# Kernel tuning notes

Hardware: AMD Instinct MI355X
Metric: run time of the kernel (lower is better)

## Reference

```python
import jax, jax.numpy as jnp
import numpy as np

EPS = 1e-06

def _hermite_coeffs(coord_diff, sigmas):
    # coord_diff: [B,N,K,2], sigmas: [K] -> coeff: [B,N,K,6]
    dx = coord_diff[..., 0]  # [B,N,K]
    dy = coord_diff[..., 1]
    s2 = sigmas ** 2 + EPS   # [K], broadcasts over B,N
    s4 = sigmas ** 4 + EPS
    ones = jnp.ones_like(dx)
    # idx order follows nested (order, alpha) loop of the torch code:
    # (0,0), (0,1)->-dy, (1,0)->-dx, (0,2), (1,1), (2,0)
    coeff = jnp.stack([
        ones,
        -dy / s2,
        -dx / s2,
        dy ** 2 / s4 - 1.0 / s2,
        dx * dy / s4,
        dx ** 2 / s4 - 1.0 / s2,
    ], axis=-1)  # [B,N,K,6]
    return coeff


def setup_inputs() -> dict:
    key = jax.random.key(0)
    k1, k2, k3, k4, k5 = jax.random.split(key, 5)
    B, N, K, H, O = 4, 65536, 32, 6, 31
    return {
        "mlp_output": jax.random.normal(k1, (B, N, O), dtype=jnp.float32),
        "coord_diff": jax.random.normal(k2, (B, N, K, 2), dtype=jnp.float32),
        "sigmas": jax.random.uniform(k3, (K,), dtype=jnp.float32, minval=0.1, maxval=1.0),
        "gaussian_weights": jax.random.uniform(k4, (B, N, K), dtype=jnp.float32),
        "rbf_weights": jax.random.normal(k5, (K, H, O), dtype=jnp.float32),
    }


def reference(mlp_output, coord_diff, sigmas, gaussian_weights, rbf_weights):
    # final[b,n,o] = mlp_output[b,n,o] * sum_{k,h} coeff[b,n,k,h]*gw[b,n,k]*W[k,h,o]
    coeff = _hermite_coeffs(coord_diff, sigmas)            # [B,N,K,6]
    mix = jnp.einsum('bnkh,bnk,kho->bno', coeff, gaussian_weights, rbf_weights)
    return mlp_output * mix
```

## Files before the change

kernel.cpp:

```cpp
#include <hip/hip_runtime.h>

#define KK 32
#define HH 6
#define OO 31
#define OP 32
#define KT 8
#define EPS 1e-6f

#define W_DW (KK * HH * OP)
#define PTS_BLK 512
#define MIX_DW (PTS_BLK * OO)

__global__ __launch_bounds__(256, 2) void hermite_fused_kernel(
    const float* __restrict__ mlp,
    const float* __restrict__ cd,
    const float* __restrict__ sigmas,
    const float* __restrict__ gw,
    const float* __restrict__ W,
    float* __restrict__ out,
    int P)
{
    __shared__ float smem[MIX_DW];
    __shared__ float s_i2[KK];
    __shared__ float s_i4[KK];

    const int tid = threadIdx.x;
    if (tid < KK) {
        float s = sigmas[tid];
        s_i2[tid] = 1.0f / (s * s + EPS);
        s_i4[tid] = 1.0f / (s * s * s * s + EPS);
    }

    for (int j = tid; j < W_DW; j += 256) {
        int k = j / (HH * OP);
        int r = j - k * (HH * OP);
        int h = r >> 5;
        int o = r & 31;
        smem[j] = (o < OO) ? W[k * (HH * OO) + h * OO + o] : 0.0f;
    }
    __syncthreads();

    const int pA = blockIdx.x * PTS_BLK + tid;
    const float4* __restrict__ cdA = (const float4*)(cd + (size_t)pA * (KK * 2));
    const float4* __restrict__ cdB = cdA + (256 * KK * 2) / 4;
    const float4* __restrict__ gwA = (const float4*)(gw + (size_t)pA * KK);
    const float4* __restrict__ gwB = gwA + (256 * KK) / 4;

    float accA[OP], accB[OP];
#pragma unroll
    for (int o = 0; o < OP; ++o) { accA[o] = 0.0f; accB[o] = 0.0f; }

#pragma unroll 1
    for (int kt = 0; kt < KK / KT; ++kt) {
        float cA[KT * 2], cB[KT * 2], gA[KT], gB[KT];
#pragma unroll
        for (int i = 0; i < KT / 2; ++i) {
            float4 t = cdA[kt * (KT / 2) + i];
            cA[4 * i + 0] = t.x; cA[4 * i + 1] = t.y; cA[4 * i + 2] = t.z; cA[4 * i + 3] = t.w;
        }
#pragma unroll
        for (int i = 0; i < KT / 2; ++i) {
            float4 t = cdB[kt * (KT / 2) + i];
            cB[4 * i + 0] = t.x; cB[4 * i + 1] = t.y; cB[4 * i + 2] = t.z; cB[4 * i + 3] = t.w;
        }
#pragma unroll
        for (int i = 0; i < KT / 4; ++i) {
            float4 t = gwA[kt * (KT / 4) + i];
            gA[4 * i + 0] = t.x; gA[4 * i + 1] = t.y; gA[4 * i + 2] = t.z; gA[4 * i + 3] = t.w;
        }
#pragma unroll
        for (int i = 0; i < KT / 4; ++i) {
            float4 t = gwB[kt * (KT / 4) + i];
            gB[4 * i + 0] = t.x; gB[4 * i + 1] = t.y; gB[4 * i + 2] = t.z; gB[4 * i + 3] = t.w;
        }

#pragma unroll
        for (int j = 0; j < KT; ++j) {
            const int k = kt * KT + j;
            float i2 = s_i2[k];
            float i4 = s_i4[k];

            float dxA = cA[2 * j], dyA = cA[2 * j + 1], ga = gA[j];
            float t2A = ga * i2, t4A = ga * i4;
            float dxt4A = dxA * t4A, dyt4A = dyA * t4A;
            float d0A = ga;
            float d1A = -dyA * t2A;
            float d2A = -dxA * t2A;
            float d3A = fmaf(dyA, dyt4A, -t2A);
            float d4A = dxA * dyt4A;
            float d5A = fmaf(dxA, dxt4A, -t2A);

            float dxB = cB[2 * j], dyB = cB[2 * j + 1], gb = gB[j];
            float t2B = gb * i2, t4B = gb * i4;
            float dxt4B = dxB * t4B, dyt4B = dyB * t4B;
            float d0B = gb;
            float d1B = -dyB * t2B;
            float d2B = -dxB * t2B;
            float d3B = fmaf(dyB, dyt4B, -t2B);
            float d4B = dxB * dyt4B;
            float d5B = fmaf(dxB, dxt4B, -t2B);

            const float4* Wk = (const float4*)&smem[k * (HH * OP)];
#pragma unroll
            for (int oq = 0; oq < OP / 4; ++oq) {
                float4 w0 = Wk[0 * (OP / 4) + oq];
                float4 w1 = Wk[1 * (OP / 4) + oq];
                float4 w2 = Wk[2 * (OP / 4) + oq];
                float4 w3 = Wk[3 * (OP / 4) + oq];
                float4 w4 = Wk[4 * (OP / 4) + oq];
                float4 w5 = Wk[5 * (OP / 4) + oq];
#define HFMA(ACC, D0, D1, D2, D3, D4, D5, C)            \
                {   float a = ACC;                      \
                    a = fmaf(D0, w0.C, a);              \
                    a = fmaf(D1, w1.C, a);              \
                    a = fmaf(D2, w2.C, a);              \
                    a = fmaf(D3, w3.C, a);              \
                    a = fmaf(D4, w4.C, a);              \
                    a = fmaf(D5, w5.C, a);              \
                    ACC = a; }
                HFMA(accA[4 * oq + 0], d0A, d1A, d2A, d3A, d4A, d5A, x)
                HFMA(accA[4 * oq + 1], d0A, d1A, d2A, d3A, d4A, d5A, y)
                HFMA(accA[4 * oq + 2], d0A, d1A, d2A, d3A, d4A, d5A, z)
                HFMA(accA[4 * oq + 3], d0A, d1A, d2A, d3A, d4A, d5A, w)
                HFMA(accB[4 * oq + 0], d0B, d1B, d2B, d3B, d4B, d5B, x)
                HFMA(accB[4 * oq + 1], d0B, d1B, d2B, d3B, d4B, d5B, y)
                HFMA(accB[4 * oq + 2], d0B, d1B, d2B, d3B, d4B, d5B, z)
                HFMA(accB[4 * oq + 3], d0B, d1B, d2B, d3B, d4B, d5B, w)
#undef HFMA
            }
        }
    }

    __syncthreads();
#pragma unroll
    for (int o = 0; o < OO; ++o) {
        smem[tid * OO + o] = accA[o];
        smem[(tid + 256) * OO + o] = accB[o];
    }
    __syncthreads();

    {
        const size_t blk_dw = (size_t)blockIdx.x * MIX_DW;
        const float4* __restrict__ mlpv = (const float4*)(mlp + blk_dw);
        float4* __restrict__ outv = (float4*)(out + blk_dw);
        const float4* mixv = (const float4*)smem;
#pragma unroll 4
        for (int j = tid; j < MIX_DW / 4; j += 256) {
            float4 m = mlpv[j];
            float4 x = mixv[j];
            float4 r;
            r.x = m.x * x.x;
            r.y = m.y * x.y;
            r.z = m.z * x.z;
            r.w = m.w * x.w;
            outv[j] = r;
        }
    }
}

extern "C" void kernel_launch(void* const* d_in, const int* in_sizes, int n_in,
                              void* d_out, int out_size, void* d_ws, size_t ws_size,
                              hipStream_t stream) {
    const float* mlp    = (const float*)d_in[0];
    const float* cd     = (const float*)d_in[1];
    const float* sigmas = (const float*)d_in[2];
    const float* gw     = (const float*)d_in[3];
    const float* W      = (const float*)d_in[4];
    float* out          = (float*)d_out;

    const int P = in_sizes[3] / KK;
    const int grid = P / PTS_BLK;

    hermite_fused_kernel<<<grid, 256, 0, stream>>>(mlp, cd, sigmas, gw, W, out, P);
}
```

Baseline: 207.2 us.

## Fold sigma scaling into prepped weights and stream them via scalar loads

Adds a small prep kernel that folds the 1/s2 and 1/s4 factors, and the constant -1/s2 terms, into a reordered weight table held in device global memory. That cuts the per-point coefficient work to a few multiplies. The main kernel now reads the weights through uniform s_load_dwordx16 scalar loads instead of LDS float4 reads. It also processes one point per thread with 256 points per block, raises launch bounds to 4 blocks per SM, and uses nontemporal loads and stores in the epilogue. The cost is an extra kernel launch and a scalar-cache wait (s_waitcnt) inside the inner loop, which may stall.

Measured after the change: 199.3 us. -3.8%, faster.

```diff
diff --git a/kernel.cpp b/kernel.cpp
--- a/kernel.cpp
+++ b/kernel.cpp
@@ -3,164 +3,149 @@
 #define KK 32
 #define HH 6
 #define OO 31
-#define OP 32
-#define KT 8
 #define EPS 1e-6f
+#define PTS_BLK 256
+#define V_DW (KK * 4 * HH * 8)
 
-#define W_DW (KK * HH * OP)
-#define PTS_BLK 512
-#define MIX_DW (PTS_BLK * OO)
+typedef float f32x16 __attribute__((ext_vector_type(16)));
+typedef float f32x4  __attribute__((ext_vector_type(4)));
 
-__global__ __launch_bounds__(256, 2) void hermite_fused_kernel(
+__device__ __align__(256) float V_dev[V_DW];
+
+__global__ void hermite_prep_kernel(const float* __restrict__ W,
+                                    const float* __restrict__ sigmas)
+{
+    int j = blockIdx.x * 256 + threadIdx.x;
+    if (j >= V_DW) return;
+    int k  = j / 192;
+    int r  = j - k * 192;
+    int oc = r / 48;
+    int r2 = r - oc * 48;
+    int h  = r2 >> 3;
+    int o  = oc * 8 + (r2 & 7);
+    float s  = sigmas[k];
+    float s2 = s * s;
+    float i2 = 1.0f / (s2 + EPS);
+    float i4 = 1.0f / (s2 * s2 + EPS);
+    float v = 0.0f;
+    if (o < OO) {
+        const float* Wk = W + k * (HH * OO);
+        float w = Wk[h * OO + o];
+        if (h == 0)      v = w - i2 * (Wk[3 * OO + o] + Wk[5 * OO + o]);
+        else if (h <= 2) v = -i2 * w;
+        else             v = i4 * w;
+    }
+    V_dev[j] = v;
+}
+
+#define CHUNK(PC, OCB)                                                     \
+    {                                                                      \
+        f32x16 t0, t1, t2;                                                 \
+        asm volatile("s_load_dwordx16 %0, %3, 0x0\n\t"                     \
+                     "s_load_dwordx16 %1, %3, 0x40\n\t"                    \
+                     "s_load_dwordx16 %2, %3, 0x80\n\t"                    \
+                     "s_waitcnt lgkmcnt(0)"                                \
+                     : "=&s"(t0), "=&s"(t1), "=&s"(t2)                     \
+                     : "s"(PC));                                           \
+        _Pragma("unroll")                                                  \
+        for (int o = 0; o < 8; ++o) {                                      \
+            float a = acc[(OCB) + o];                                      \
+            a = fmaf(g,  t0[o],     a);                                    \
+            a = fmaf(d1, t0[8 + o], a);                                    \
+            a = fmaf(d2, t1[o],     a);                                    \
+            a = fmaf(d3, t1[8 + o], a);                                    \
+            a = fmaf(d4, t2[o],     a);                                    \
+            a = fmaf(d5, t2[8 + o], a);                                    \
+            acc[(OCB) + o] = a;                                            \
+        }                                                                  \
+    }
+
+#define JBLOCK(VS, GOFF)                                                   \
+    _Pragma("unroll")                                                      \
+    for (int j = 0; j < 8; ++j) {                                          \
+        float dx = c[2 * j], dy = c[2 * j + 1];                            \
+        float g  = ga[(GOFF) + j];                                         \
+        float d1 = g * dy, d2 = g * dx;                                    \
+        float d3 = d1 * dy, d4 = d1 * dx, d5 = d2 * dx;                    \
+        const float* pk = (VS) + j * 192;                                  \
+        CHUNK(pk,        0)                                                \
+        CHUNK(pk + 48,   8)                                                \
+        CHUNK(pk + 96,  16)                                                \
+        CHUNK(pk + 144, 24)                                                \
+    }
+
+__global__ __launch_bounds__(256, 4) void hermite_fused_kernel(
     const float* __restrict__ mlp,
     const float* __restrict__ cd,
-    const float* __restrict__ sigmas,
     const float* __restrict__ gw,
-    const float* __restrict__ W,
-    float* __restrict__ out,
-    int P)
+    float* __restrict__ out)
 {
-    __shared__ float smem[MIX_DW];
-    __shared__ float s_i2[KK];
-    __shared__ float s_i4[KK];
+    __shared__ float smem[PTS_BLK * OO];
 
     const int tid = threadIdx.x;
-    if (tid < KK) {
-        float s = sigmas[tid];
-        s_i2[tid] = 1.0f / (s * s + EPS);
-        s_i4[tid] = 1.0f / (s * s * s * s + EPS);
+    const int p   = blockIdx.x * PTS_BLK + tid;
+    const float4* __restrict__ cdv = (const float4*)(cd + (size_t)p * (KK * 2));
+    const float4* __restrict__ gwv = (const float4*)(gw + (size_t)p * KK);
+
+    float acc[32];
+#pragma unroll
+    for (int o = 0; o < 32; ++o) acc[o] = 0.0f;
+
+    const float* __restrict__ Vb = V_dev;
+
+#pragma unroll 1
+    for (int kt2 = 0; kt2 < 2; ++kt2) {
+        float ga[16];
+#pragma unroll
+        for (int i = 0; i < 4; ++i) {
+            float4 t = gwv[kt2 * 4 + i];
+            ga[4 * i + 0] = t.x; ga[4 * i + 1] = t.y;
+            ga[4 * i + 2] = t.z; ga[4 * i + 3] = t.w;
+        }
+
+        float c[16];
+#pragma unroll
+        for (int i = 0; i < 4; ++i) {
+            float4 t = cdv[kt2 * 8 + i];
+            c[4 * i + 0] = t.x; c[4 * i + 1] = t.y;
+            c[4 * i + 2] = t.z; c[4 * i + 3] = t.w;
+        }
+        const float* Vs0 = Vb + (size_t)kt2 * (16 * 192);
+        JBLOCK(Vs0, 0)
+
+#pragma unroll
+        for (int i = 0; i < 4; ++i) {
+            float4 t = cdv[kt2 * 8 + 4 + i];
+            c[4 * i + 0] = t.x; c[4 * i + 1] = t.y;
+            c[4 * i + 2] = t.z; c[4 * i + 3] = t.w;
+        }
+        const float* Vs1 = Vs0 + 8 * 192;
+        JBLOCK(Vs1, 8)
     }
 
-    for (int j = tid; j < W_DW; j += 256) {
-        int k = j / (HH * OP);
-        int r = j - k * (HH * OP);
-        int h = r >> 5;
-        int o = r & 31;
-        smem[j] = (o < OO) ? W[k * (HH * OO) + h * OO + o] : 0.0f;
-    }
-    __syncthreads();
-
-    const int pA = blockIdx.x * PTS_BLK + tid;
-    const float4* __restrict__ cdA = (const float4*)(cd + (size_t)pA * (KK * 2));
-    const float4* __restrict__ cdB = cdA + (256 * KK * 2) / 4;
-    const float4* __restrict__ gwA = (const float4*)(gw + (size_t)pA * KK);
-    const float4* __restrict__ gwB = gwA + (256 * KK) / 4;
-
-    float accA[OP], accB[OP];
 #pragma unroll
-    for (int o = 0; o < OP; ++o) { accA[o] = 0.0f; accB[o] = 0.0f; }
-
-#pragma unroll 1
-    for (int kt = 0; kt < KK / KT; ++kt) {
-        float cA[KT * 2], cB[KT * 2], gA[KT], gB[KT];
-#pragma unroll
-        for (int i = 0; i < KT / 2; ++i) {
-            float4 t = cdA[kt * (KT / 2) + i];
-            cA[4 * i + 0] = t.x; cA[4 * i + 1] = t.y; cA[4 * i + 2] = t.z; cA[4 * i + 3] = t.w;
-        }
-#pragma unroll
-        for (int i = 0; i < KT / 2; ++i) {
-            float4 t = cdB[kt * (KT / 2) + i];
-            cB[4 * i + 0] = t.x; cB[4 * i + 1] = t.y; cB[4 * i + 2] = t.z; cB[4 * i + 3] = t.w;
-        }
-#pragma unroll
-        for (int i = 0; i < KT / 4; ++i) {
-            float4 t = gwA[kt * (KT / 4) + i];
-            gA[4 * i + 0] = t.x; gA[4 * i + 1] = t.y; gA[4 * i + 2] = t.z; gA[4 * i + 3] = t.w;
-        }
-#pragma unroll
-        for (int i = 0; i < KT / 4; ++i) {
-            float4 t = gwB[kt * (KT / 4) + i];
-            gB[4 * i + 0] = t.x; gB[4 * i + 1] = t.y; gB[4 * i + 2] = t.z; gB[4 * i + 3] = t.w;
-        }
-
-#pragma unroll
-        for (int j = 0; j < KT; ++j) {
-            const int k = kt * KT + j;
-            float i2 = s_i2[k];
-            float i4 = s_i4[k];
-
-            float dxA = cA[2 * j], dyA = cA[2 * j + 1], ga = gA[j];
-            float t2A = ga * i2, t4A = ga * i4;
-            float dxt4A = dxA * t4A, dyt4A = dyA * t4A;
-            float d0A = ga;
-            float d1A = -dyA * t2A;
-            float d2A = -dxA * t2A;
-            float d3A = fmaf(dyA, dyt4A, -t2A);
-            float d4A = dxA * dyt4A;
-            float d5A = fmaf(dxA, dxt4A, -t2A);
-
-            float dxB = cB[2 * j], dyB = cB[2 * j + 1], gb = gB[j];
-            float t2B = gb * i2, t4B = gb * i4;
-            float dxt4B = dxB * t4B, dyt4B = dyB * t4B;
-            float d0B = gb;
-            float d1B = -dyB * t2B;
-            float d2B = -dxB * t2B;
-            float d3B = fmaf(dyB, dyt4B, -t2B);
-            float d4B = dxB * dyt4B;
-            float d5B = fmaf(dxB, dxt4B, -t2B);
-
-            const float4* Wk = (const float4*)&smem[k * (HH * OP)];
-#pragma unroll
-            for (int oq = 0; oq < OP / 4; ++oq) {
-                float4 w0 = Wk[0 * (OP / 4) + oq];
-                float4 w1 = Wk[1 * (OP / 4) + oq];
-                float4 w2 = Wk[2 * (OP / 4) + oq];
-                float4 w3 = Wk[3 * (OP / 4) + oq];
-                float4 w4 = Wk[4 * (OP / 4) + oq];
-                float4 w5 = Wk[5 * (OP / 4) + oq];
-#define HFMA(ACC, D0, D1, D2, D3, D4, D5, C)            \
-                {   float a = ACC;                      \
-                    a = fmaf(D0, w0.C, a);              \
-                    a = fmaf(D1, w1.C, a);              \
-                    a = fmaf(D2, w2.C, a);              \
-                    a = fmaf(D3, w3.C, a);              \
-                    a = fmaf(D4, w4.C, a);              \
-                    a = fmaf(D5, w5.C, a);              \
-                    ACC = a; }
-                HFMA(accA[4 * oq + 0], d0A, d1A, d2A, d3A, d4A, d5A, x)
-                HFMA(accA[4 * oq + 1], d0A, d1A, d2A, d3A, d4A, d5A, y)
-                HFMA(accA[4 * oq + 2], d0A, d1A, d2A, d3A, d4A, d5A, z)
-                HFMA(accA[4 * oq + 3], d0A, d1A, d2A, d3A, d4A, d5A, w)
-                HFMA(accB[4 * oq + 0], d0B, d1B, d2B, d3B, d4B, d5B, x)
-                HFMA(accB[4 * oq + 1], d0B, d1B, d2B, d3B, d4B, d5B, y)
-                HFMA(accB[4 * oq + 2], d0B, d1B, d2B, d3B, d4B, d5B, z)
-                HFMA(accB[4 * oq + 3], d0B, d1B, d2B, d3B, d4B, d5B, w)
-#undef HFMA
-            }
-        }
-    }
-
-    __syncthreads();
-#pragma unroll
-    for (int o = 0; o < OO; ++o) {
-        smem[tid * OO + o] = accA[o];
-        smem[(tid + 256) * OO + o] = accB[o];
-    }
+    for (int o = 0; o < OO; ++o) smem[tid * OO + o] = acc[o];
     __syncthreads();
 
     {
-        const size_t blk_dw = (size_t)blockIdx.x * MIX_DW;
-        const float4* __restrict__ mlpv = (const float4*)(mlp + blk_dw);
-        float4* __restrict__ outv = (float4*)(out + blk_dw);
-        const float4* mixv = (const float4*)smem;
-#pragma unroll 4
-        for (int j = tid; j < MIX_DW / 4; j += 256) {
-            float4 m = mlpv[j];
-            float4 x = mixv[j];
-            float4 r;
-            r.x = m.x * x.x;
-            r.y = m.y * x.y;
-            r.z = m.z * x.z;
-            r.w = m.w * x.w;
-            outv[j] = r;
+        const size_t blk_dw = (size_t)blockIdx.x * (PTS_BLK * OO);
+        const f32x4* __restrict__ mlpv = (const f32x4*)(mlp + blk_dw);
+        f32x4* __restrict__ outv = (f32x4*)(out + blk_dw);
+        const f32x4* mixv = (const f32x4*)smem;
+#pragma unroll 2
+        for (int j = tid; j < (PTS_BLK * OO) / 4; j += 256) {
+            f32x4 m = __builtin_nontemporal_load(&mlpv[j]);
+            f32x4 x = mixv[j];
+            f32x4 r = m * x;
+            __builtin_nontemporal_store(r, &outv[j]);
         }
     }
 }
 
 extern "C" void kernel_launch(void* const* d_in, const int* in_sizes, int n_in,
                               void* d_out, int out_size, void* d_ws, size_t ws_size,
-                              hipStream_t stream) {
+                              hipStream_t stream)
+{
     const float* mlp    = (const float*)d_in[0];
     const float* cd     = (const float*)d_in[1];
     const float* sigmas = (const float*)d_in[2];
@@ -169,7 +154,7 @@
     float* out          = (float*)d_out;
 
     const int P = in_sizes[3] / KK;
-    const int grid = P / PTS_BLK;
 
-    hermite_fused_kernel<<<grid, 256, 0, stream>>>(mlp, cd, sigmas, gw, W, out, P);
+    hermite_prep_kernel<<<(V_DW + 255) / 256, 256, 0, stream>>>(W, sigmas);
+    hermite_fused_kernel<<<P / PTS_BLK, 256, 0, stream>>>(mlp, cd, gw, out);
 }
```
